# Kernel optimization log

Hardware: AMD Instinct MI355X
Metric: run time of the kernel (lower is better)

## Reference

```python
import jax, jax.numpy as jnp
import numpy as np
import math

D_MODEL = 768
EXPAND = 2
D_INNER = D_MODEL * EXPAND  # 1536
D_CONV = 4
D_STATE = 16
DT_RANK = math.ceil(D_MODEL / 16)  # 48
B, L = 2, 2048
LN_EPS = 1e-5


def setup_inputs() -> dict:
    key = jax.random.key(0)
    ks = jax.random.split(key, 12)
    s = lambda fan_in: 1.0 / np.sqrt(fan_in)
    return {
        "x": jax.random.normal(ks[0], (B, L, D_MODEL), dtype=jnp.float32),
        "ln_w": jnp.ones((D_MODEL,), jnp.float32),
        "ln_b": jnp.zeros((D_MODEL,), jnp.float32),
        "in_proj_w": jax.random.normal(ks[1], (2 * D_INNER, D_MODEL), jnp.float32) * s(D_MODEL),
        "conv_w": jax.random.normal(ks[2], (D_INNER, D_CONV), jnp.float32) * s(D_CONV),
        "conv_b": jax.random.normal(ks[3], (D_INNER,), jnp.float32) * 0.01,
        "x_proj_w": jax.random.normal(ks[4], (DT_RANK + 2 * D_STATE, D_INNER), jnp.float32) * s(D_INNER),
        "dt_proj_w": jax.random.normal(ks[5], (D_INNER, DT_RANK), jnp.float32) * s(DT_RANK),
        "dt_proj_b": jax.random.normal(ks[6], (D_INNER,), jnp.float32) * 0.01,
        "A_log": jnp.log(jnp.broadcast_to(jnp.arange(1, D_STATE + 1, dtype=jnp.float32), (D_INNER, D_STATE))),
        "D": jnp.ones((D_INNER,), jnp.float32),
        "out_proj_w": jax.random.normal(ks[7], (D_MODEL, D_INNER), jnp.float32) * s(D_INNER),
    }


def _layernorm(x, w, b):
    mu = jnp.mean(x, axis=-1, keepdims=True)
    var = jnp.mean(jnp.square(x - mu), axis=-1, keepdims=True)
    return (x - mu) * jax.lax.rsqrt(var + LN_EPS) * w + b


def _selective_scan(u, delta, A, Bm, Cm, Dv):
    # u,delta: [b,l,d]; A: [d,n]; Bm,Cm: [b,l,n]; Dv: [d]
    deltaA = jnp.exp(delta[..., None] * A)               # [b,l,d,n]
    dBu = (delta * u)[..., None] * Bm[:, :, None, :]     # [b,l,d,n]
    b, l, d, n = deltaA.shape
    x0 = jnp.zeros((b, d, n), deltaA.dtype)

    def step(carry, inp):
        dA_i, dBu_i, C_i = inp                            # [b,d,n],[b,d,n],[b,n]
        x_new = dA_i * carry + dBu_i
        y_i = jnp.einsum('bdn,bn->bd', x_new, C_i)
        return x_new, y_i

    _, ys = jax.lax.scan(
        step, x0,
        (deltaA.transpose(1, 0, 2, 3), dBu.transpose(1, 0, 2, 3), Cm.transpose(1, 0, 2)))
    y = ys.transpose(1, 0, 2)                             # [b,l,d]
    return y + u * Dv


def reference(x, ln_w, ln_b, in_proj_w, conv_w, conv_b, x_proj_w,
              dt_proj_w, dt_proj_b, A_log, D, out_proj_w):
    residual = x
    h = _layernorm(x, ln_w, ln_b)
    xr = h @ in_proj_w.T                                  # [b,l,2*d_inner]
    u, res = jnp.split(xr, [D_INNER], axis=-1)
    # depthwise causal conv1d
    uc = u.transpose(0, 2, 1)                             # [b,d,l]
    uc = jax.lax.conv_general_dilated(
        uc, conv_w[:, None, :], window_strides=(1,),
        padding=[(D_CONV - 1, 0)],
        dimension_numbers=('NCH', 'OIH', 'NCH'),
        feature_group_count=D_INNER) + conv_b[None, :, None]
    u = jax.nn.silu(uc.transpose(0, 2, 1))                # [b,l,d]
    # SSM
    x_dbl = u @ x_proj_w.T
    dt, Bm, Cm = jnp.split(x_dbl, [DT_RANK, DT_RANK + D_STATE], axis=-1)
    delta = jax.nn.softplus(dt @ dt_proj_w.T + dt_proj_b)
    A = -jnp.exp(A_log)
    y = _selective_scan(u, delta, A, Bm, Cm, D)
    y = y * jax.nn.silu(res)
    return y @ out_proj_w.T + residual
```

## Files before the change

### kernel.cpp

```cpp
#include <hip/hip_runtime.h>

#define DEV __device__ __forceinline__

typedef __attribute__((ext_vector_type(8))) short bf16x8;
typedef __attribute__((ext_vector_type(4))) float f32x4;

#define BB 2
#define LL 2048
#define MM 4096
#define DMODEL 768
#define DINNER 1536
#define NSTATE 16
#define CH 32
#define NCH 64

DEV unsigned short f2b(float f) {
  unsigned int x = __float_as_uint(f);
  x += 0x7fffu + ((x >> 16) & 1u);
  return (unsigned short)(x >> 16);
}
DEV float b2f(unsigned short u) { return __uint_as_float(((unsigned int)u) << 16); }
DEV float silu_f(float v) { return v / (1.f + __expf(-v)); }

DEV void async16(void* lds, const void* g) {
  __builtin_amdgcn_global_load_lds(
      (const __attribute__((address_space(1))) unsigned int*)g,
      (__attribute__((address_space(3))) unsigned int*)lds, 16, 0, 0);
}

__global__ __launch_bounds__(256) void k_prep(const float* __restrict__ w_in,
                                              const float* __restrict__ w_out,
                                              const float* __restrict__ w_xp,
                                              const float* __restrict__ w_dt,
                                              const float* __restrict__ alog,
                                              unsigned short* __restrict__ winb,
                                              unsigned short* __restrict__ woutb,
                                              unsigned short* __restrict__ wxpb,
                                              unsigned short* __restrict__ wdtb,
                                              float* __restrict__ a2) {
  int bid = blockIdx.x, t = threadIdx.x;
  if (bid < 2304) {
    int i = bid * 256 + t;
    float4 v = ((const float4*)w_in)[i];
    ushort4 o; o.x = f2b(v.x); o.y = f2b(v.y); o.z = f2b(v.z); o.w = f2b(v.w);
    ((ushort4*)winb)[i] = o;
  } else if (bid < 3456) {
    int i = (bid - 2304) * 256 + t;
    float4 v = ((const float4*)w_out)[i];
    ushort4 o; o.x = f2b(v.x); o.y = f2b(v.y); o.z = f2b(v.z); o.w = f2b(v.w);
    ((ushort4*)woutb)[i] = o;
  } else if (bid < 4224) {
    int i = (bid - 3456) * 256 + t;
    wxpb[i] = (i < 80 * 1536) ? f2b(w_xp[i]) : (unsigned short)0;
  } else if (bid < 4608) {
    int i = (bid - 4224) * 256 + t;
    int row = i >> 6, col = i & 63;
    wdtb[i] = (col < 48) ? f2b(w_dt[row * 48 + col]) : (unsigned short)0;
  } else {
    int i = (bid - 4608) * 256 + t;
    a2[i] = -__expf(alog[i]) * 1.44269504088896f;
  }
}

__global__ __launch_bounds__(256) void k_ln(const float* __restrict__ x,
                                            const float* __restrict__ w,
                                            const float* __restrict__ b,
                                            unsigned short* __restrict__ h) {
  int row = blockIdx.x, tid = threadIdx.x;
  const float* xr = x + (size_t)row * DMODEL;
  float v0 = xr[tid], v1 = xr[tid + 256], v2 = xr[tid + 512];
  float s = v0 + v1 + v2;
  float s2 = v0 * v0 + v1 * v1 + v2 * v2;
#pragma unroll
  for (int o = 32; o > 0; o >>= 1) { s += __shfl_down(s, o); s2 += __shfl_down(s2, o); }
  __shared__ float ps[4], ps2[4];
  if ((tid & 63) == 0) { ps[tid >> 6] = s; ps2[tid >> 6] = s2; }
  __syncthreads();
  s = ps[0] + ps[1] + ps[2] + ps[3];
  s2 = ps2[0] + ps2[1] + ps2[2] + ps2[3];
  float mu = s * (1.f / DMODEL);
  float var = s2 * (1.f / DMODEL) - mu * mu;
  float rs = rsqrtf(var + 1e-5f);
  h[(size_t)row * DMODEL + tid]       = f2b((v0 - mu) * rs * w[tid] + b[tid]);
  h[(size_t)row * DMODEL + tid + 256] = f2b((v1 - mu) * rs * w[tid + 256] + b[tid + 256]);
  h[(size_t)row * DMODEL + tid + 512] = f2b((v2 - mu) * rs * w[tid + 512] + b[tid + 512]);
}

template <int EPI, int OBF>
__global__ __launch_bounds__(256) void k_gemm_bt(const unsigned short* __restrict__ A,
                                                 const unsigned short* __restrict__ B,
                                                 float* __restrict__ C,
                                                 unsigned short* __restrict__ Cb,
                                                 int M, int N, int Kst, int KC,
                                                 const float* __restrict__ aux) {
  __shared__ unsigned short lA[128 * 32];
  __shared__ unsigned short lB[128 * 32];
  const int tid = threadIdx.x;
  const int bm = blockIdx.x * 128;
  const int bn = blockIdx.y * 128;
  const int lane = tid & 63;
  const int w = tid >> 6;
  const int wr = (w >> 1) * 64;
  const int wc = (w & 1) * 64;

  f32x4 acc[4][4];
#pragma unroll
  for (int i = 0; i < 4; ++i)
#pragma unroll
    for (int j = 0; j < 4; ++j) acc[i][j] = (f32x4)(0.0f);

  const int srow = tid >> 2;
  const int sg = ((tid & 3) ^ ((srow >> 2) & 3)) * 8;
  const int k0 = blockIdx.z * KC;

  for (int kt = k0; kt < k0 + KC; kt += 32) {
#pragma unroll
    for (int s = 0; s < 2; ++s) {
      int row = s * 64 + srow;
      int f = s * 256 + tid;
      async16(&lA[f * 8], A + (size_t)(bm + row) * Kst + kt + sg);
      async16(&lB[f * 8], B + (size_t)(bn + row) * Kst + kt + sg);
    }
    __syncthreads();
    const int ll = lane & 15, sl = lane >> 4;
    bf16x8 af[4], bfr[4];
#pragma unroll
    for (int mi = 0; mi < 4; ++mi) {
      int row = wr + mi * 16 + ll;
      af[mi] = *(const bf16x8*)&lA[row * 32 + ((sl ^ ((row >> 2) & 3)) * 8)];
    }
#pragma unroll
    for (int ni = 0; ni < 4; ++ni) {
      int row = wc + ni * 16 + ll;
      bfr[ni] = *(const bf16x8*)&lB[row * 32 + ((sl ^ ((row >> 2) & 3)) * 8)];
    }
#pragma unroll
    for (int mi = 0; mi < 4; ++mi)
#pragma unroll
      for (int ni = 0; ni < 4; ++ni)
        acc[mi][ni] = __builtin_amdgcn_mfma_f32_16x16x32_bf16(af[mi], bfr[ni], acc[mi][ni], 0, 0, 0);
    __syncthreads();
  }

  const size_t zoff = (size_t)blockIdx.z * M * N;
  const int ll = lane & 15, lh4 = (lane >> 4) * 4;
#pragma unroll
  for (int mi = 0; mi < 4; ++mi) {
#pragma unroll
    for (int ni = 0; ni < 4; ++ni) {
      int col = bn + wc + ni * 16 + ll;
#pragma unroll
      for (int q = 0; q < 4; ++q) {
        int row = bm + wr + mi * 16 + lh4 + q;
        size_t idx = (size_t)row * N + col;
        float v = acc[mi][ni][q];
        if (EPI == 1) { v += aux[col]; v = (v > 20.f) ? v : __logf(1.f + __expf(v)); }
        if (OBF) Cb[idx] = f2b(v);
        else C[zoff + idx] = v;
      }
    }
  }
}

__global__ __launch_bounds__(256) void k_gemm64(const unsigned short* __restrict__ A,
                                                const unsigned short* __restrict__ B,
                                                float* __restrict__ C,
                                                int M, int N, int Kst, int KC) {
  __shared__ unsigned short lA[64 * 32];
  __shared__ unsigned short lB[128 * 32];
  const int tid = threadIdx.x;
  const int bm = blockIdx.x * 64;
  const int bn = blockIdx.y * 128;
  const int lane = tid & 63;
  const int w = tid >> 6;
  const int wr = (w >> 1) * 32;
  const int wc = (w & 1) * 64;

  f32x4 acc[2][4];
#pragma unroll
  for (int i = 0; i < 2; ++i)
#pragma unroll
    for (int j = 0; j < 4; ++j) acc[i][j] = (f32x4)(0.0f);

  const int srow = tid >> 2;
  const int sg = ((tid & 3) ^ ((srow >> 2) & 3)) * 8;
  const int k0 = blockIdx.z * KC;

  for (int kt = k0; kt < k0 + KC; kt += 32) {
    async16(&lA[tid * 8], A + (size_t)(bm + srow) * Kst + kt + sg);
#pragma unroll
    for (int i = 0; i < 2; ++i) {
      int f = i * 256 + tid;
      int r = f >> 2;
      int g = ((f & 3) ^ ((r >> 2) & 3)) * 8;
      async16(&lB[f * 8], B + (size_t)(bn + r) * Kst + kt + g);
    }
    __syncthreads();
    const int ll = lane & 15, sl = lane >> 4;
    bf16x8 af[2], bfr[4];
#pragma unroll
    for (int mi = 0; mi < 2; ++mi) {
      int row = wr + mi * 16 + ll;
      af[mi] = *(const bf16x8*)&lA[row * 32 + ((sl ^ ((row >> 2) & 3)) * 8)];
    }
#pragma unroll
    for (int ni = 0; ni < 4; ++ni) {
      int row = wc + ni * 16 + ll;
      bfr[ni] = *(const bf16x8*)&lB[row * 32 + ((sl ^ ((row >> 2) & 3)) * 8)];
    }
#pragma unroll
    for (int mi = 0; mi < 2; ++mi)
#pragma unroll
      for (int ni = 0; ni < 4; ++ni)
        acc[mi][ni] = __builtin_amdgcn_mfma_f32_16x16x32_bf16(af[mi], bfr[ni], acc[mi][ni], 0, 0, 0);
    __syncthreads();
  }

  const size_t zoff = (size_t)blockIdx.z * M * N;
  const int ll = lane & 15, lh4 = (lane >> 4) * 4;
#pragma unroll
  for (int mi = 0; mi < 2; ++mi) {
#pragma unroll
    for (int ni = 0; ni < 4; ++ni) {
      int col = bn + wc + ni * 16 + ll;
#pragma unroll
      for (int q = 0; q < 4; ++q) {
        int row = bm + wr + mi * 16 + lh4 + q;
        C[zoff + (size_t)row * N + col] = acc[mi][ni][q];
      }
    }
  }
}

__global__ __launch_bounds__(128) void k_xpj_fin(const float* __restrict__ part,
                                                 float* __restrict__ xdbl,
                                                 unsigned short* __restrict__ dtb) {
  int row = blockIdx.x, t = threadIdx.x;
  size_t idx = (size_t)row * 128 + t;
  float s = 0.f;
#pragma unroll
  for (int p = 0; p < 8; ++p) s += part[(size_t)p * MM * 128 + idx];
  xdbl[idx] = s;
  if (t < 64) dtb[row * 64 + t] = (t < 48) ? f2b(s) : (unsigned short)0;
}

__global__ __launch_bounds__(256) void k_opj_fin(const float* __restrict__ part,
                                                 const float* __restrict__ x,
                                                 float* __restrict__ out) {
  int i = blockIdx.x * 256 + threadIdx.x;
  f32x4 a = ((const f32x4*)part)[i];
  f32x4 b = ((const f32x4*)(part + (size_t)MM * DMODEL))[i];
  f32x4 r = ((const f32x4*)x)[i];
  ((f32x4*)out)[i] = a + b + r;
}

__global__ __launch_bounds__(256) void k_conv(const unsigned short* __restrict__ xrb,
                                              const float* __restrict__ cw,
                                              const float* __restrict__ cb,
                                              unsigned short* __restrict__ ub) {
  int i = blockIdx.x * 256 + threadIdx.x;
  int d4 = i % (DINNER / 4);
  int m = i / (DINNER / 4);
  int l = m & (LL - 1);
  const f32x4* cw4 = (const f32x4*)cw;
  f32x4 w0 = cw4[d4 * 4 + 0], w1 = cw4[d4 * 4 + 1];
  f32x4 w2 = cw4[d4 * 4 + 2], w3 = cw4[d4 * 4 + 3];
  f32x4 acc = ((const f32x4*)cb)[d4];
#pragma unroll
  for (int j = 0; j < 4; ++j) {
    if (l - 3 + j >= 0) {
      ushort4 in = ((const ushort4*)(xrb + (size_t)(m - 3 + j) * 3072))[d4];
      f32x4 iv;
      iv[0] = b2f(in.x); iv[1] = b2f(in.y); iv[2] = b2f(in.z); iv[3] = b2f(in.w);
      f32x4 wj;
      wj[0] = w0[j]; wj[1] = w1[j]; wj[2] = w2[j]; wj[3] = w3[j];
      acc += iv * wj;
    }
  }
  ushort4 ob;
  ob.x = f2b(silu_f(acc[0])); ob.y = f2b(silu_f(acc[1]));
  ob.z = f2b(silu_f(acc[2])); ob.w = f2b(silu_f(acc[3]));
  ((ushort4*)ub)[i] = ob;
}

__global__ __launch_bounds__(256) void k_scan1(const unsigned short* __restrict__ deltab,
                                               const unsigned short* __restrict__ ub,
                                               const float* __restrict__ xdbl,
                                               const float* __restrict__ a2g,
                                               float* __restrict__ P, float* __restrict__ S) {
  __shared__ unsigned short sd[CH * 256];
  __shared__ unsigned short su[CH * 256];
  int bid = blockIdx.x;
  int dblk = bid % 6;
  int c = (bid / 6) % NCH;
  int b = bid / (6 * NCH);
  int t = threadIdx.x;
  int d0 = dblk * 256, d = d0 + t;
  size_t mbase = (size_t)b * LL + c * CH;
#pragma unroll
  for (int i = 0; i < 4; ++i) {
    int o = i * 256 + t, r = o >> 5, l = o & 31;
    async16(&sd[r * 256 + l * 8], deltab + (mbase + r) * DINNER + d0 + l * 8);
    async16(&su[r * 256 + l * 8], ub + (mbase + r) * DINNER + d0 + l * 8);
  }
  f32x4 a2v[4], xs[4], pr[4];
  const f32x4* ga = (const f32x4*)(a2g + (size_t)d * 16);
#pragma unroll
  for (int q = 0; q < 4; ++q) { a2v[q] = ga[q]; xs[q] = (f32x4)(0.f); pr[q] = (f32x4)(1.f); }
  __syncthreads();

#pragma unroll 4
  for (int s = 0; s < CH; ++s) {
    float dt = b2f(sd[s * 256 + t]);
    float du = dt * b2f(su[s * 256 + t]);
    const f32x4* gb = (const f32x4*)(xdbl + (mbase + s) * 128 + 48);
#pragma unroll
    for (int q = 0; q < 4; ++q) {
      f32x4 bv = gb[q];
      f32x4 e = dt * a2v[q];
      f32x4 dA;
#pragma unroll
      for (int k = 0; k < 4; ++k) dA[k] = __builtin_amdgcn_exp2f(e[k]);
      xs[q] = dA * xs[q] + du * bv;
      pr[q] = pr[q] * dA;
    }
  }
  size_t base = (size_t)(b * NCH + c) * (16 * DINNER) + d;
#pragma unroll
  for (int q = 0; q < 4; ++q)
#pragma unroll
    for (int k = 0; k < 4; ++k) {
      P[base + (size_t)(q * 4 + k) * DINNER] = pr[q][k];
      S[base + (size_t)(q * 4 + k) * DINNER] = xs[q][k];
    }
}

__global__ __launch_bounds__(256) void k_scan2(float* __restrict__ P, const float* __restrict__ S) {
  int i = blockIdx.x * 256 + threadIdx.x;
  int b = i / (DINNER * 16);
  int j = i % (DINNER * 16);
  const size_t cs = (size_t)DINNER * 16;
  float* Pp = P + (size_t)b * NCH * cs + j;
  const float* Sp = S + (size_t)b * NCH * cs + j;
  float p0[8], s0[8], p1[8], s1[8];
#pragma unroll
  for (int k = 0; k < 8; ++k) { p0[k] = Pp[(size_t)k * cs]; s0[k] = Sp[(size_t)k * cs]; }
#pragma unroll
  for (int k = 0; k < 8; ++k) { p1[k] = Pp[(size_t)(8 + k) * cs]; s1[k] = Sp[(size_t)(8 + k) * cs]; }
  float carry = 0.f;
  for (int g = 0; g < NCH / 8; ++g) {
    float np[8], ns[8];
#pragma unroll
    for (int k = 0; k < 8; ++k) { np[k] = 0.f; ns[k] = 0.f; }
    if (g + 2 < NCH / 8) {
#pragma unroll
      for (int k = 0; k < 8; ++k) {
        np[k] = Pp[(size_t)((g + 2) * 8 + k) * cs];
        ns[k] = Sp[(size_t)((g + 2) * 8 + k) * cs];
      }
    }
#pragma unroll
    for (int k = 0; k < 8; ++k) {
      float tmp = carry;
      carry = fmaf(p0[k], carry, s0[k]);
      Pp[(size_t)(g * 8 + k) * cs] = tmp;
    }
#pragma unroll
    for (int k = 0; k < 8; ++k) { p0[k] = p1[k]; s0[k] = s1[k]; p1[k] = np[k]; s1[k] = ns[k]; }
  }
}

__global__ __launch_bounds__(256) void k_scan3(const unsigned short* __restrict__ deltab,
                                               const unsigned short* __restrict__ ub,
                                               const float* __restrict__ xdbl,
                                               const float* __restrict__ a2g,
                                               const float* __restrict__ P,
                                               const float* __restrict__ Dv,
                                               const unsigned short* __restrict__ xrb,
                                               unsigned short* __restrict__ yb) {
  __shared__ unsigned short sd[CH * 256];
  __shared__ unsigned short su[CH * 256];
  int bid = blockIdx.x;
  int dblk = bid % 6;
  int c = (bid / 6) % NCH;
  int b = bid / (6 * NCH);
  int t = threadIdx.x;
  int d0 = dblk * 256, d = d0 + t;
  size_t mbase = (size_t)b * LL + c * CH;
#pragma unroll
  for (int i = 0; i < 4; ++i) {
    int o = i * 256 + t, r = o >> 5, l = o & 31;
    async16(&sd[r * 256 + l * 8], deltab + (mbase + r) * DINNER + d0 + l * 8);
    async16(&su[r * 256 + l * 8], ub + (mbase + r) * DINNER + d0 + l * 8);
  }
  f32x4 a2v[4], xs[4];
  const f32x4* ga = (const f32x4*)(a2g + (size_t)d * 16);
#pragma unroll
  for (int q = 0; q < 4; ++q) a2v[q] = ga[q];
  size_t base = (size_t)(b * NCH + c) * (16 * DINNER) + d;
#pragma unroll
  for (int q = 0; q < 4; ++q)
#pragma unroll
    for (int k = 0; k < 4; ++k) xs[q][k] = P[base + (size_t)(q * 4 + k) * DINNER];
  float dval = Dv[d];
  __syncthreads();

#pragma unroll 4
  for (int s = 0; s < CH; ++s) {
    size_t m = mbase + s;
    float dt = b2f(sd[s * 256 + t]);
    float uv = b2f(su[s * 256 + t]);
    float du = dt * uv;
    const f32x4* gb = (const f32x4*)(xdbl + m * 128 + 48);
    const f32x4* gc = (const f32x4*)(xdbl + m * 128 + 64);
    f32x4 yv = (f32x4)(0.f);
#pragma unroll
    for (int q = 0; q < 4; ++q) {
      f32x4 bv = gb[q], cv = gc[q];
      f32x4 e = dt * a2v[q];
      f32x4 dA;
#pragma unroll
      for (int k = 0; k < 4; ++k) dA[k] = __builtin_amdgcn_exp2f(e[k]);
      xs[q] = dA * xs[q] + du * bv;
      yv += xs[q] * cv;
    }
    float y = yv[0] + yv[1] + yv[2] + yv[3] + uv * dval;
    float res = b2f(xrb[m * 3072 + DINNER + d]);
    y *= silu_f(res);
    yb[m * DINNER + d] = f2b(y);
  }
}

extern "C" void kernel_launch(void* const* d_in, const int* in_sizes, int n_in,
                              void* d_out, int out_size, void* d_ws, size_t ws_size,
                              hipStream_t stream) {
  const float* x     = (const float*)d_in[0];
  const float* ln_w  = (const float*)d_in[1];
  const float* ln_b  = (const float*)d_in[2];
  const float* w_in  = (const float*)d_in[3];
  const float* cw    = (const float*)d_in[4];
  const float* cb    = (const float*)d_in[5];
  const float* w_xp  = (const float*)d_in[6];
  const float* w_dt  = (const float*)d_in[7];
  const float* b_dt  = (const float*)d_in[8];
  const float* alog  = (const float*)d_in[9];
  const float* Dv    = (const float*)d_in[10];
  const float* w_out = (const float*)d_in[11];
  float* out = (float*)d_out;

  char* ws = (char*)d_ws;
  unsigned short* h_b    = (unsigned short*)(ws + 0);
  unsigned short* winb   = (unsigned short*)(ws + 6291456);
  unsigned short* woutb  = (unsigned short*)(ws + 11010048);
  unsigned short* wxpb   = (unsigned short*)(ws + 13369344);
  unsigned short* wdtb   = (unsigned short*)(ws + 13762560);
  float*          a2     = (float*)(ws + 13959168);
  unsigned short* xrb    = (unsigned short*)(ws + 14057472);
  unsigned short* ub     = (unsigned short*)(ws + 39223296);
  float*          xpart  = (float*)(ws + 51806208);
  float*          xdbl   = (float*)(ws + 68583424);
  unsigned short* dtb    = (unsigned short*)(ws + 70680576);
  unsigned short* deltab = (unsigned short*)(ws + 71204864);
  float*          P      = (float*)(ws + 83787776);
  float*          S      = (float*)(ws + 96370688);
  unsigned short* yb     = (unsigned short*)(ws + 108953600);
  float*          opart  = (float*)(ws + 121536512);

  k_prep<<<4704, 256, 0, stream>>>(w_in, w_out, w_xp, w_dt, alog, winb, woutb, wxpb, wdtb, a2);

  k_ln<<<MM, 256, 0, stream>>>(x, ln_w, ln_b, h_b);

  k_gemm_bt<0, 1><<<dim3(32, 24, 1), 256, 0, stream>>>(h_b, winb, nullptr, xrb, MM, 3072, 768, 768, nullptr);

  k_conv<<<(MM * (DINNER / 4)) / 256, 256, 0, stream>>>(xrb, cw, cb, ub);

  k_gemm_bt<0, 0><<<dim3(32, 1, 8), 256, 0, stream>>>(ub, wxpb, xpart, nullptr, MM, 128, 1536, 192, nullptr);
  k_xpj_fin<<<MM, 128, 0, stream>>>(xpart, xdbl, dtb);

  k_gemm_bt<1, 1><<<dim3(32, 12, 1), 256, 0, stream>>>(dtb, wdtb, nullptr, deltab, MM, DINNER, 64, 64, b_dt);

  k_scan1<<<BB * NCH * 6, 256, 0, stream>>>(deltab, ub, xdbl, a2, P, S);
  k_scan2<<<(BB * DINNER * 16) / 256, 256, 0, stream>>>(P, S);
  k_scan3<<<BB * NCH * 6, 256, 0, stream>>>(deltab, ub, xdbl, a2, P, Dv, xrb, yb);

  k_gemm64<<<dim3(64, 6, 2), 256, 0, stream>>>(yb, woutb, opart, MM, DMODEL, 1536, 768);
  k_opj_fin<<<(MM * DMODEL / 4) / 256, 256, 0, stream>>>(opart, x, out);
}
```

Before: 164.8 us.

## Double-buffer GEMM LDS tiles, remap blocks across XCDs, fuse layernorm into prep

Both GEMM kernels now use two LDS buffers: the next K-tile is loaded asynchronously while MFMAs run on the current one, with a single waitcnt and barrier per iteration. The grids become 1D, and block IDs are permuted so that groups of 8 consecutive blocks map to contiguous tiles, meant to improve L2 locality across XCDs. The layernorm kernel is merged into the weight-conversion prep kernel to save one launch. LDS use doubles, which may lower occupancy, and the wait still drains all outstanding loads every iteration.

```diff
diff --git a/kernel.cpp b/kernel.cpp
--- a/kernel.cpp
+++ b/kernel.cpp
@@ -28,17 +28,43 @@
       (__attribute__((address_space(3))) unsigned int*)lds, 16, 0, 0);
 }
 
-__global__ __launch_bounds__(256) void k_prep(const float* __restrict__ w_in,
-                                              const float* __restrict__ w_out,
-                                              const float* __restrict__ w_xp,
-                                              const float* __restrict__ w_dt,
-                                              const float* __restrict__ alog,
-                                              unsigned short* __restrict__ winb,
-                                              unsigned short* __restrict__ woutb,
-                                              unsigned short* __restrict__ wxpb,
-                                              unsigned short* __restrict__ wdtb,
-                                              float* __restrict__ a2) {
-  int bid = blockIdx.x, t = threadIdx.x;
+__global__ __launch_bounds__(256) void k_prepln(const float* __restrict__ x,
+                                                const float* __restrict__ ln_w,
+                                                const float* __restrict__ ln_b,
+                                                unsigned short* __restrict__ h,
+                                                const float* __restrict__ w_in,
+                                                const float* __restrict__ w_out,
+                                                const float* __restrict__ w_xp,
+                                                const float* __restrict__ w_dt,
+                                                const float* __restrict__ alog,
+                                                unsigned short* __restrict__ winb,
+                                                unsigned short* __restrict__ woutb,
+                                                unsigned short* __restrict__ wxpb,
+                                                unsigned short* __restrict__ wdtb,
+                                                float* __restrict__ a2) {
+  int bid0 = blockIdx.x, t = threadIdx.x;
+  if (bid0 < 4096) {
+    int row = bid0;
+    const float* xr = x + (size_t)row * DMODEL;
+    float v0 = xr[t], v1 = xr[t + 256], v2 = xr[t + 512];
+    float s = v0 + v1 + v2;
+    float s2 = v0 * v0 + v1 * v1 + v2 * v2;
+#pragma unroll
+    for (int o = 32; o > 0; o >>= 1) { s += __shfl_down(s, o); s2 += __shfl_down(s2, o); }
+    __shared__ float ps[4], ps2[4];
+    if ((t & 63) == 0) { ps[t >> 6] = s; ps2[t >> 6] = s2; }
+    __syncthreads();
+    s = ps[0] + ps[1] + ps[2] + ps[3];
+    s2 = ps2[0] + ps2[1] + ps2[2] + ps2[3];
+    float mu = s * (1.f / DMODEL);
+    float var = s2 * (1.f / DMODEL) - mu * mu;
+    float rs = rsqrtf(var + 1e-5f);
+    h[(size_t)row * DMODEL + t]       = f2b((v0 - mu) * rs * ln_w[t] + ln_b[t]);
+    h[(size_t)row * DMODEL + t + 256] = f2b((v1 - mu) * rs * ln_w[t + 256] + ln_b[t + 256]);
+    h[(size_t)row * DMODEL + t + 512] = f2b((v2 - mu) * rs * ln_w[t + 512] + ln_b[t + 512]);
+    return;
+  }
+  int bid = bid0 - 4096;
   if (bid < 2304) {
     int i = bid * 256 + t;
     float4 v = ((const float4*)w_in)[i];
@@ -62,42 +88,23 @@
   }
 }
 
-__global__ __launch_bounds__(256) void k_ln(const float* __restrict__ x,
-                                            const float* __restrict__ w,
-                                            const float* __restrict__ b,
-                                            unsigned short* __restrict__ h) {
-  int row = blockIdx.x, tid = threadIdx.x;
-  const float* xr = x + (size_t)row * DMODEL;
-  float v0 = xr[tid], v1 = xr[tid + 256], v2 = xr[tid + 512];
-  float s = v0 + v1 + v2;
-  float s2 = v0 * v0 + v1 * v1 + v2 * v2;
-#pragma unroll
-  for (int o = 32; o > 0; o >>= 1) { s += __shfl_down(s, o); s2 += __shfl_down(s2, o); }
-  __shared__ float ps[4], ps2[4];
-  if ((tid & 63) == 0) { ps[tid >> 6] = s; ps2[tid >> 6] = s2; }
-  __syncthreads();
-  s = ps[0] + ps[1] + ps[2] + ps[3];
-  s2 = ps2[0] + ps2[1] + ps2[2] + ps2[3];
-  float mu = s * (1.f / DMODEL);
-  float var = s2 * (1.f / DMODEL) - mu * mu;
-  float rs = rsqrtf(var + 1e-5f);
-  h[(size_t)row * DMODEL + tid]       = f2b((v0 - mu) * rs * w[tid] + b[tid]);
-  h[(size_t)row * DMODEL + tid + 256] = f2b((v1 - mu) * rs * w[tid + 256] + b[tid + 256]);
-  h[(size_t)row * DMODEL + tid + 512] = f2b((v2 - mu) * rs * w[tid + 512] + b[tid + 512]);
-}
-
 template <int EPI, int OBF>
 __global__ __launch_bounds__(256) void k_gemm_bt(const unsigned short* __restrict__ A,
                                                  const unsigned short* __restrict__ B,
                                                  float* __restrict__ C,
                                                  unsigned short* __restrict__ Cb,
                                                  int M, int N, int Kst, int KC,
+                                                 int NBN, int NBM,
                                                  const float* __restrict__ aux) {
-  __shared__ unsigned short lA[128 * 32];
-  __shared__ unsigned short lB[128 * 32];
+  __shared__ unsigned short lA[2][128 * 32];
+  __shared__ unsigned short lB[2][128 * 32];
   const int tid = threadIdx.x;
-  const int bm = blockIdx.x * 128;
-  const int bn = blockIdx.y * 128;
+  const int nwg = gridDim.x;
+  const int sid = (blockIdx.x & 7) * (nwg >> 3) + (blockIdx.x >> 3);
+  const int bn = (sid % NBN) * 128;
+  const int t2 = sid / NBN;
+  const int bm = (t2 % NBM) * 128;
+  const int z = t2 / NBM;
   const int lane = tid & 63;
   const int w = tid >> 6;
   const int wr = (w >> 1) * 64;
@@ -111,38 +118,50 @@
 
   const int srow = tid >> 2;
   const int sg = ((tid & 3) ^ ((srow >> 2) & 3)) * 8;
-  const int k0 = blockIdx.z * KC;
-
-  for (int kt = k0; kt < k0 + KC; kt += 32) {
-#pragma unroll
-    for (int s = 0; s < 2; ++s) {
-      int row = s * 64 + srow;
-      int f = s * 256 + tid;
-      async16(&lA[f * 8], A + (size_t)(bm + row) * Kst + kt + sg);
-      async16(&lB[f * 8], B + (size_t)(bn + row) * Kst + kt + sg);
-    }
-    __syncthreads();
+  const int k0 = z * KC;
+
+#define STAGE_BT(buf, kt)                                                   \
+  do {                                                                      \
+    _Pragma("unroll") for (int s_ = 0; s_ < 2; ++s_) {                      \
+      int row_ = s_ * 64 + srow;                                            \
+      int f_ = s_ * 256 + tid;                                              \
+      async16(&lA[buf][f_ * 8], A + (size_t)(bm + row_) * Kst + (kt) + sg); \
+      async16(&lB[buf][f_ * 8], B + (size_t)(bn + row_) * Kst + (kt) + sg); \
+    }                                                                       \
+  } while (0)
+
+  STAGE_BT(0, k0);
+  asm volatile("s_waitcnt vmcnt(0)" ::: "memory");
+  __builtin_amdgcn_s_barrier();
+
+  const int nt = KC >> 5;
+  int cur = 0;
+  for (int t = 0; t < nt; ++t) {
+    if (t + 1 < nt) STAGE_BT(cur ^ 1, k0 + (t + 1) * 32);
     const int ll = lane & 15, sl = lane >> 4;
     bf16x8 af[4], bfr[4];
 #pragma unroll
     for (int mi = 0; mi < 4; ++mi) {
       int row = wr + mi * 16 + ll;
-      af[mi] = *(const bf16x8*)&lA[row * 32 + ((sl ^ ((row >> 2) & 3)) * 8)];
+      af[mi] = *(const bf16x8*)&lA[cur][row * 32 + ((sl ^ ((row >> 2) & 3)) * 8)];
     }
 #pragma unroll
     for (int ni = 0; ni < 4; ++ni) {
       int row = wc + ni * 16 + ll;
-      bfr[ni] = *(const bf16x8*)&lB[row * 32 + ((sl ^ ((row >> 2) & 3)) * 8)];
+      bfr[ni] = *(const bf16x8*)&lB[cur][row * 32 + ((sl ^ ((row >> 2) & 3)) * 8)];
     }
 #pragma unroll
     for (int mi = 0; mi < 4; ++mi)
 #pragma unroll
       for (int ni = 0; ni < 4; ++ni)
         acc[mi][ni] = __builtin_amdgcn_mfma_f32_16x16x32_bf16(af[mi], bfr[ni], acc[mi][ni], 0, 0, 0);
-    __syncthreads();
-  }
-
-  const size_t zoff = (size_t)blockIdx.z * M * N;
+    asm volatile("s_waitcnt vmcnt(0)" ::: "memory");
+    __builtin_amdgcn_s_barrier();
+    cur ^= 1;
+  }
+#undef STAGE_BT
+
+  const size_t zoff = (size_t)z * M * N;
   const int ll = lane & 15, lh4 = (lane >> 4) * 4;
 #pragma unroll
   for (int mi = 0; mi < 4; ++mi) {
@@ -165,12 +184,17 @@
 __global__ __launch_bounds__(256) void k_gemm64(const unsigned short* __restrict__ A,
                                                 const unsigned short* __restrict__ B,
                                                 float* __restrict__ C,
-                                                int M, int N, int Kst, int KC) {
-  __shared__ unsigned short lA[64 * 32];
-  __shared__ unsigned short lB[128 * 32];
+                                                int M, int N, int Kst, int KC,
+                                                int NBN, int NBM) {
+  __shared__ unsigned short lA[2][64 * 32];
+  __shared__ unsigned short lB[2][128 * 32];
   const int tid = threadIdx.x;
-  const int bm = blockIdx.x * 64;
-  const int bn = blockIdx.y * 128;
+  const int nwg = gridDim.x;
+  const int sid = (blockIdx.x & 7) * (nwg >> 3) + (blockIdx.x >> 3);
+  const int bn = (sid % NBN) * 128;
+  const int t2 = sid / NBN;
+  const int bm = (t2 % NBM) * 64;
+  const int z = t2 / NBM;
   const int lane = tid & 63;
   const int w = tid >> 6;
   const int wr = (w >> 1) * 32;
@@ -184,39 +208,51 @@
 
   const int srow = tid >> 2;
   const int sg = ((tid & 3) ^ ((srow >> 2) & 3)) * 8;
-  const int k0 = blockIdx.z * KC;
-
-  for (int kt = k0; kt < k0 + KC; kt += 32) {
-    async16(&lA[tid * 8], A + (size_t)(bm + srow) * Kst + kt + sg);
-#pragma unroll
-    for (int i = 0; i < 2; ++i) {
-      int f = i * 256 + tid;
-      int r = f >> 2;
-      int g = ((f & 3) ^ ((r >> 2) & 3)) * 8;
-      async16(&lB[f * 8], B + (size_t)(bn + r) * Kst + kt + g);
-    }
-    __syncthreads();
+  const int k0 = z * KC;
+
+#define STAGE_64(buf, kt)                                                    \
+  do {                                                                       \
+    async16(&lA[buf][tid * 8], A + (size_t)(bm + srow) * Kst + (kt) + sg);   \
+    _Pragma("unroll") for (int i_ = 0; i_ < 2; ++i_) {                       \
+      int f_ = i_ * 256 + tid;                                               \
+      int r_ = f_ >> 2;                                                      \
+      int g_ = ((f_ & 3) ^ ((r_ >> 2) & 3)) * 8;                             \
+      async16(&lB[buf][f_ * 8], B + (size_t)(bn + r_) * Kst + (kt) + g_);    \
+    }                                                                        \
+  } while (0)
+
+  STAGE_64(0, k0);
+  asm volatile("s_waitcnt vmcnt(0)" ::: "memory");
+  __builtin_amdgcn_s_barrier();
+
+  const int nt = KC >> 5;
+  int cur = 0;
+  for (int t = 0; t < nt; ++t) {
+    if (t + 1 < nt) STAGE_64(cur ^ 1, k0 + (t + 1) * 32);
     const int ll = lane & 15, sl = lane >> 4;
     bf16x8 af[2], bfr[4];
 #pragma unroll
     for (int mi = 0; mi < 2; ++mi) {
       int row = wr + mi * 16 + ll;
-      af[mi] = *(const bf16x8*)&lA[row * 32 + ((sl ^ ((row >> 2) & 3)) * 8)];
+      af[mi] = *(const bf16x8*)&lA[cur][row * 32 + ((sl ^ ((row >> 2) & 3)) * 8)];
     }
 #pragma unroll
     for (int ni = 0; ni < 4; ++ni) {
       int row = wc + ni * 16 + ll;
-      bfr[ni] = *(const bf16x8*)&lB[row * 32 + ((sl ^ ((row >> 2) & 3)) * 8)];
+      bfr[ni] = *(const bf16x8*)&lB[cur][row * 32 + ((sl ^ ((row >> 2) & 3)) * 8)];
     }
 #pragma unroll
     for (int mi = 0; mi < 2; ++mi)
 #pragma unroll
       for (int ni = 0; ni < 4; ++ni)
         acc[mi][ni] = __builtin_amdgcn_mfma_f32_16x16x32_bf16(af[mi], bfr[ni], acc[mi][ni], 0, 0, 0);
-    __syncthreads();
-  }
-
-  const size_t zoff = (size_t)blockIdx.z * M * N;
+    asm volatile("s_waitcnt vmcnt(0)" ::: "memory");
+    __builtin_amdgcn_s_barrier();
+    cur ^= 1;
+  }
+#undef STAGE_64
+
+  const size_t zoff = (size_t)z * M * N;
   const int ll = lane & 15, lh4 = (lane >> 4) * 4;
 #pragma unroll
   for (int mi = 0; mi < 2; ++mi) {
@@ -466,23 +502,22 @@
   unsigned short* yb     = (unsigned short*)(ws + 108953600);
   float*          opart  = (float*)(ws + 121536512);
 
-  k_prep<<<4704, 256, 0, stream>>>(w_in, w_out, w_xp, w_dt, alog, winb, woutb, wxpb, wdtb, a2);
-
-  k_ln<<<MM, 256, 0, stream>>>(x, ln_w, ln_b, h_b);
-
-  k_gemm_bt<0, 1><<<dim3(32, 24, 1), 256, 0, stream>>>(h_b, winb, nullptr, xrb, MM, 3072, 768, 768, nullptr);
+  k_prepln<<<8800, 256, 0, stream>>>(x, ln_w, ln_b, h_b, w_in, w_out, w_xp, w_dt, alog,
+                                     winb, woutb, wxpb, wdtb, a2);
+
+  k_gemm_bt<0, 1><<<768, 256, 0, stream>>>(h_b, winb, nullptr, xrb, MM, 3072, 768, 768, 24, 32, nullptr);
 
   k_conv<<<(MM * (DINNER / 4)) / 256, 256, 0, stream>>>(xrb, cw, cb, ub);
 
-  k_gemm_bt<0, 0><<<dim3(32, 1, 8), 256, 0, stream>>>(ub, wxpb, xpart, nullptr, MM, 128, 1536, 192, nullptr);
+  k_gemm_bt<0, 0><<<256, 256, 0, stream>>>(ub, wxpb, xpart, nullptr, MM, 128, 1536, 192, 1, 32, nullptr);
   k_xpj_fin<<<MM, 128, 0, stream>>>(xpart, xdbl, dtb);
 
-  k_gemm_bt<1, 1><<<dim3(32, 12, 1), 256, 0, stream>>>(dtb, wdtb, nullptr, deltab, MM, DINNER, 64, 64, b_dt);
+  k_gemm_bt<1, 1><<<384, 256, 0, stream>>>(dtb, wdtb, nullptr, deltab, MM, DINNER, 64, 64, 12, 32, b_dt);
 
   k_scan1<<<BB * NCH * 6, 256, 0, stream>>>(deltab, ub, xdbl, a2, P, S);
   k_scan2<<<(BB * DINNER * 16) / 256, 256, 0, stream>>>(P, S);
   k_scan3<<<BB * NCH * 6, 256, 0, stream>>>(deltab, ub, xdbl, a2, P, Dv, xrb, yb);
 
-  k_gemm64<<<dim3(64, 6, 2), 256, 0, stream>>>(yb, woutb, opart, MM, DMODEL, 1536, 768);
+  k_gemm64<<<768, 256, 0, stream>>>(yb, woutb, opart, MM, DMODEL, 1536, 768, 6, 64);
   k_opj_fin<<<(MM * DMODEL / 4) / 256, 256, 0, stream>>>(opart, x, out);
 }
```

After: 161.9 us. Within noise of the previous version (-1.8%).
